# Optimization experiments

Hardware: AMD Instinct MI355X
Metric: run time of the kernel (lower is better)

## Reference

```python
import jax, jax.numpy as jnp
import numpy as np

ND, NT = 30000, 15000
FD, FT = 200, 570
H = 768
E_DD, E_DT, E_TT = 300000, 400000, 200000
NEG_SLOPE = 0.2


def _gat(x_src, x_dst, src, dst, Ws, Wd, a_s, a_d, b, n_dst):
    # PyG GATConv, heads=1: hs = lin_src(x_src), hd = lin_dst(x_dst)
    hs = x_src @ Ws                       # [Ns, H]
    hd = x_dst @ Wd                       # [Nd, H]
    es = hs @ a_s                         # [Ns]
    ed = hd @ a_d                         # [Nd]
    e = jax.nn.leaky_relu(es[src] + ed[dst], negative_slope=NEG_SLOPE)  # [E]
    m = jax.ops.segment_max(e, dst, num_segments=n_dst)
    m = jnp.where(jnp.isfinite(m), m, 0.0)
    w = jnp.exp(e - m[dst])
    s = jax.ops.segment_sum(w, dst, num_segments=n_dst)
    alpha = w / (s[dst] + 1e-16)
    out = jax.ops.segment_sum(hs[src] * alpha[:, None], dst, num_segments=n_dst)  # [n_dst, H]
    return out + b


def _layer(xd, xt, dd_src, dd_dst, dt_src, dt_dst, tt_src, tt_dst, p):
    nd, nt = xd.shape[0], xt.shape[0]
    sl_d = jnp.arange(nd, dtype=dd_src.dtype)
    sl_t = jnp.arange(nt, dtype=tt_src.dtype)
    # add_self_loops=True for the homogeneous relations d-d and t-t
    dds = jnp.concatenate([dd_src, sl_d]); ddd = jnp.concatenate([dd_dst, sl_d])
    tts = jnp.concatenate([tt_src, sl_t]); ttd = jnp.concatenate([tt_dst, sl_t])
    o_dd = _gat(xd, xd, dds, ddd, p['Wsrc_dd'], p['Wdst_dd'], p['asrc_dd'], p['adst_dd'], p['b_dd'], nd)
    o_rv = _gat(xt, xd, dt_dst, dt_src, p['Wsrc_rv'], p['Wdst_rv'], p['asrc_rv'], p['adst_rv'], p['b_rv'], nd)
    o_dt = _gat(xd, xt, dt_src, dt_dst, p['Wsrc_dt'], p['Wdst_dt'], p['asrc_dt'], p['adst_dt'], p['b_dt'], nt)
    o_tt = _gat(xt, xt, tts, ttd, p['Wsrc_tt'], p['Wdst_tt'], p['asrc_tt'], p['adst_tt'], p['b_tt'], nt)
    # HeteroConv aggr='sum', then relu per node type
    return jax.nn.relu(o_dd + o_rv), jax.nn.relu(o_dt + o_tt)


def setup_inputs() -> dict:
    key = jax.random.key(0)
    ks = jax.random.split(key, 40)
    d = {}
    d['drug_x'] = jax.random.normal(ks[0], (ND, FD), jnp.float32)
    d['target_x'] = jax.random.normal(ks[1], (NT, FT), jnp.float32)
    d['dd_src'] = jax.random.randint(ks[2], (E_DD,), 0, ND, jnp.int32)
    d['dd_dst'] = jax.random.randint(ks[3], (E_DD,), 0, ND, jnp.int32)
    d['dt_src'] = jax.random.randint(ks[4], (E_DT,), 0, ND, jnp.int32)
    d['dt_dst'] = jax.random.randint(ks[5], (E_DT,), 0, NT, jnp.int32)
    d['tt_src'] = jax.random.randint(ks[6], (E_TT,), 0, NT, jnp.int32)
    d['tt_dst'] = jax.random.randint(ks[7], (E_TT,), 0, NT, jnp.int32)
    d['drug_mask'] = jax.random.randint(ks[8], (ND, 1), 0, 2, jnp.int32)
    d['target_mask'] = jax.random.randint(ks[9], (NT, 1), 0, 2, jnp.int32)
    d['mask_drug'] = 0.05 * jax.random.normal(ks[10], (1, FD), jnp.float32)
    d['mask_target'] = 0.05 * jax.random.normal(ks[11], (1, FT), jnp.float32)
    i = 12
    for rel, fin_s, fin_d in [('dd', FD, FD), ('dt', FD, FT), ('rv', FT, FD), ('tt', FT, FT)]:
        d['Wsrc_' + rel] = 0.05 * jax.random.normal(ks[i], (fin_s, H), jnp.float32); i += 1
        d['Wdst_' + rel] = 0.05 * jax.random.normal(ks[i], (fin_d, H), jnp.float32); i += 1
        d['asrc_' + rel] = 0.05 * jax.random.normal(ks[i], (H,), jnp.float32); i += 1
        d['adst_' + rel] = 0.05 * jax.random.normal(ks[i], (H,), jnp.float32); i += 1
        d['b_' + rel] = jnp.zeros((H,), jnp.float32)
    return d


def reference(drug_x, target_x, dd_src, dd_dst, dt_src, dt_dst, tt_src, tt_dst,
              drug_mask, target_mask, mask_drug, mask_target,
              Wsrc_dd, Wdst_dd, asrc_dd, adst_dd, b_dd,
              Wsrc_dt, Wdst_dt, asrc_dt, adst_dt, b_dt,
              Wsrc_rv, Wdst_rv, asrc_rv, adst_rv, b_rv,
              Wsrc_tt, Wdst_tt, asrc_tt, adst_tt, b_tt):
    p = dict(Wsrc_dd=Wsrc_dd, Wdst_dd=Wdst_dd, asrc_dd=asrc_dd, adst_dd=adst_dd, b_dd=b_dd,
             Wsrc_dt=Wsrc_dt, Wdst_dt=Wdst_dt, asrc_dt=asrc_dt, adst_dt=adst_dt, b_dt=b_dt,
             Wsrc_rv=Wsrc_rv, Wdst_rv=Wdst_rv, asrc_rv=asrc_rv, adst_rv=adst_rv, b_rv=b_rv,
             Wsrc_tt=Wsrc_tt, Wdst_tt=Wdst_tt, asrc_tt=asrc_tt, adst_tt=adst_tt, b_tt=b_tt)
    xd, xt = _layer(drug_x, target_x, dd_src, dd_dst, dt_src, dt_dst, tt_src, tt_dst, p)
    # MAE branch: replace masked node features with learned mask token, rerun conv
    dm = drug_mask.astype(jnp.float32)
    tm = target_mask.astype(jnp.float32)
    _dx = drug_x * (1.0 - dm) + dm * mask_drug
    _tx = target_x * (1.0 - tm) + tm * mask_target
    _xd, _xt = _layer(_dx, _tx, dd_src, dd_dst, dt_src, dt_dst, tt_src, tt_dst, p)
    loss_mae = (((xd - _xd) ** 2) * dm).sum() / (dm.sum() * H + 1e-16) \
             + (((xt - _xt) ** 2) * tm).sum() / (tm.sum() * H + 1e-16)
    return (xd, xt, loss_mae)
```

## Files before the change

kernel.cpp:

```cpp
#include <hip/hip_runtime.h>
#include <hip/hip_bf16.h>

#define ND 30000
#define NT 15000
#define FD 200
#define FT 570
#define HDIM 768
#define EDD 300000
#define EDT 400000
#define ETT 200000

#define KPD 256
#define KPT 576
#define KPA 832

#define BM 128
#define BN 128
#define GBK 32
#define KTILES (KPA / GBK)
#define MTD ((ND + BM - 1) / BM)
#define MTT ((NT + BM - 1) / BM)

typedef __attribute__((ext_vector_type(8))) short short8;
typedef __attribute__((ext_vector_type(4))) float float4v;


__device__ __forceinline__ float ldx(const void* p, size_t i, int f32) {
  return f32 ? ((const float*)p)[i]
             : __bfloat162float(((const __hip_bfloat16*)p)[i]);
}
__device__ __forceinline__ void stx(void* p, size_t i, int f32, float v) {
  if (f32) ((float*)p)[i] = v;
  else     ((__hip_bfloat16*)p)[i] = __float2bfloat16(v);
}
__device__ __forceinline__ float b2f(unsigned short u) {
  return __uint_as_float(((unsigned)u) << 16);
}
__device__ __forceinline__ unsigned short f2b(float f) {
  __hip_bfloat16 h = __float2bfloat16(f);
  return *(unsigned short*)&h;
}
__device__ __forceinline__ unsigned pk2(float a, float b) {
  return (unsigned)f2b(a) | ((unsigned)f2b(b) << 16);
}

__device__ __forceinline__ float wave_reduce(float v) {
#pragma unroll
  for (int off = 32; off > 0; off >>= 1) v += __shfl_xor(v, off, 64);
  return v;
}

__global__ void sniff(const void* x, int* flag) {
  int t = threadIdx.x;
  float cnt = 0.f;
  for (int i = t; i < 8192; i += 256) {
    float v = __bfloat162float(((const __hip_bfloat16*)x)[i]);
    if (!(fabsf(v) < 100.f)) cnt += 1.f;
  }
  cnt = wave_reduce(cnt);
  __shared__ float red[4];
  if ((t & 63) == 0) red[t >> 6] = cnt;
  __syncthreads();
  if (t == 0) flag[0] = (red[0] + red[1] + red[2] + red[3] > 256.f) ? 1 : 0;
}

__global__ __launch_bounds__(256) void wa_dot8(
    const void* W0, const void* W1, const void* W2, const void* W3,
    const void* W4, const void* W5, const void* W6, const void* W7,
    const void* a0, const void* a1, const void* a2, const void* a3,
    const void* a4, const void* a5, const void* a6, const void* a7,
    float* __restrict__ vaD, float* __restrict__ vaT,
    const int* __restrict__ flag) {
  const void* Ws[8] = {W0, W1, W2, W3, W4, W5, W6, W7};
  const void* as[8] = {a0, a1, a2, a3, a4, a5, a6, a7};
  int f32 = flag[0];
  int wid = (blockIdx.x * 256 + threadIdx.x) >> 6;
  int lane = threadIdx.x & 63;
  const void* W; const void* a; float* out; int k;
  if (wid < 4 * FD) {
    int q = wid / FD; k = wid - q * FD;
    W = Ws[q]; a = as[q]; out = vaD + q * FD + k;
  } else {
    int w2 = wid - 4 * FD;
    if (w2 >= 4 * FT) return;
    int q = w2 / FT; k = w2 - q * FT;
    W = Ws[4 + q]; a = as[4 + q]; out = vaT + q * FT + k;
  }
  float acc = 0.f;
  for (int h = lane; h < HDIM; h += 64)
    acc += ldx(W, (size_t)k * HDIM + h, f32) * ldx(a, h, f32);
  acc = wave_reduce(acc);
  if (lane == 0) *out = acc;
}

__global__ void tok_dots(const void* __restrict__ tok1, const void* __restrict__ tok2,
                         const float* __restrict__ vaD, const float* __restrict__ vaT,
                         float* __restrict__ ts, const int* __restrict__ flag) {
  int w = threadIdx.x >> 6;
  int lane = threadIdx.x & 63;
  int f32 = flag[0];
  float acc = 0.f;
  if (w < 4) {
    for (int k = lane; k < FD; k += 64) acc += ldx(tok1, k, f32) * vaD[w * FD + k];
  } else {
    int q = w - 4;
    for (int k = lane; k < FT; k += 64) acc += ldx(tok2, k, f32) * vaT[q * FT + k];
  }
  acc = wave_reduce(acc);
  if (lane == 0) {
    const int map[8] = {0, 1, 3, 4, 2, 5, 6, 7};
    ts[map[w]] = acc;
  }
}

__global__ __launch_bounds__(256) void pack_rowdot(
    const void* __restrict__ xD, const void* __restrict__ xT,
    const float* __restrict__ vaD, const float* __restrict__ vaT,
    unsigned short* __restrict__ Ad, unsigned short* __restrict__ At,
    float* __restrict__ dvec, float* __restrict__ tvec,
    const int* __restrict__ flag) {
  int wid = (blockIdx.x * 256 + threadIdx.x) >> 6;
  int lane = threadIdx.x & 63;
  int f32 = flag[0];
  const void* x; const float* va; unsigned short* Aout; float* outv; int K, Kp, row;
  if (wid < ND) { x = xD; va = vaD; Aout = Ad; outv = dvec; K = FD; Kp = KPD; row = wid; }
  else if (wid < ND + NT) { x = xT; va = vaT; Aout = At; outv = tvec; K = FT; Kp = KPT; row = wid - ND; }
  else return;
  float a0 = 0.f, a1 = 0.f, a2 = 0.f, a3 = 0.f;
  for (int it = 0; it * 256 < Kp; ++it) {
    int base = 4 * lane + it * 256;
    if (base >= Kp) continue;
    ushort4 o;
    unsigned short r[4];
    float fv[4];
#pragma unroll
    for (int c = 0; c < 4; ++c) {
      int kk = base + c;
      float f = (kk < K) ? ldx(x, (size_t)row * K + kk, f32) : 0.f;
      fv[c] = f;
      r[c] = f2b(f);
    }
    o.x = r[0]; o.y = r[1]; o.z = r[2]; o.w = r[3];
    *(ushort4*)(Aout + (size_t)row * Kp + base) = o;
#pragma unroll
    for (int c = 0; c < 4; ++c) {
      int kk = base + c;
      if (kk < K) {
        a0 += fv[c] * va[kk];
        a1 += fv[c] * va[K + kk];
        a2 += fv[c] * va[2 * K + kk];
        a3 += fv[c] * va[3 * K + kk];
      }
    }
  }
  a0 = wave_reduce(a0); a1 = wave_reduce(a1);
  a2 = wave_reduce(a2); a3 = wave_reduce(a3);
  if (lane == 0) {
    float* o = outv + (size_t)row * 4;
    o[0] = a0; o[1] = a1; o[2] = a2; o[3] = a3;
  }
}

__global__ __launch_bounds__(256) void pack_bTa2(
    const void* __restrict__ W1a, const void* __restrict__ W2a, unsigned short* __restrict__ Ba,
    const void* __restrict__ W1b, const void* __restrict__ W2b, unsigned short* __restrict__ Bb,
    const int* __restrict__ flag) {
  int f32 = flag[0];
  long long one = (long long)HDIM * KPA / 4;
  long long gid = (long long)blockIdx.x * 256 + threadIdx.x;
  if (gid >= 2 * one) return;
  const void* W1; const void* W2; unsigned short* Bout;
  if (gid < one) { W1 = W1a; W2 = W2a; Bout = Ba; }
  else { W1 = W1b; W2 = W2b; Bout = Bb; gid -= one; }
  long long e0 = gid * 4;
  int n = (int)(e0 / KPA);
  int k = (int)(e0 % KPA);
  ushort4 o;
  unsigned short r[4];
#pragma unroll
  for (int c = 0; c < 4; ++c) {
    int kk = k + c;
    float f = 0.f;
    if (kk < 256) {
      if (kk < FD) f = ldx(W1, (size_t)kk * HDIM + n, f32);
    } else {
      int k2 = kk - 256;
      if (k2 < FT) f = ldx(W2, (size_t)k2 * HDIM + n, f32);
    }
    r[c] = f2b(f);
  }
  o.x = r[0]; o.y = r[1]; o.z = r[2]; o.w = r[3];
  *(ushort4*)(Bout + e0) = o;
}

__global__ void zero_i32(int* __restrict__ p, int n) {
  int i = blockIdx.x * 256 + threadIdx.x;
  if (i < n) p[i] = 0;
}

__global__ void count4(const int* __restrict__ dd_dst, const int* __restrict__ dt_src,
                       const int* __restrict__ dt_dst, const int* __restrict__ tt_dst,
                       int* __restrict__ c_dd, int* __restrict__ c_rv,
                       int* __restrict__ c_dt, int* __restrict__ c_tt) {
  int i = blockIdx.x * 256 + threadIdx.x;
  if (i < EDD + ND) { int d = (i < EDD) ? dd_dst[i] : i - EDD; atomicAdd(&c_dd[d], 1); return; }
  i -= EDD + ND;
  if (i < EDT) { atomicAdd(&c_rv[dt_src[i]], 1); return; }
  i -= EDT;
  if (i < EDT) { atomicAdd(&c_dt[dt_dst[i]], 1); return; }
  i -= EDT;
  if (i < ETT + NT) { int d = (i < ETT) ? tt_dst[i] : i - ETT; atomicAdd(&c_tt[d], 1); }
}

__global__ __launch_bounds__(256) void scan6(
    const int* __restrict__ a0, int n0, int* __restrict__ o0,
    const int* __restrict__ a1, int n1, int* __restrict__ o1,
    const int* __restrict__ a2, int n2, int* __restrict__ o2,
    const int* __restrict__ a3, int n3, int* __restrict__ o3,
    const int* __restrict__ a4, int n4, int* __restrict__ o4,
    const int* __restrict__ a5, int n5, int* __restrict__ o5) {
  const int* a; int n; int* o;
  switch (blockIdx.x) {
    case 0: a = a0; n = n0; o = o0; break;
    case 1: a = a1; n = n1; o = o1; break;
    case 2: a = a2; n = n2; o = o2; break;
    case 3: a = a3; n = n3; o = o3; break;
    case 4: a = a4; n = n4; o = o4; break;
    default: a = a5; n = n5; o = o5; break;
  }
  __shared__ int part[256];
  int t = threadIdx.x;
  int strip = (n + 255) / 256;
  int lo = min(t * strip, n), hi = min(lo + strip, n);
  int s = 0;
  for (int i = lo; i < hi; ++i) s += a[i];
  part[t] = s;
  __syncthreads();
  if (t == 0) {
    int run = 0;
    for (int i = 0; i < 256; ++i) { int v = part[i]; part[i] = run; run += v; }
  }
  __syncthreads();
  int run = part[t];
  for (int i = lo; i < hi; ++i) { o[i] = run; run += a[i]; }
  if (hi == n) o[n] = run;
}

__global__ void ridx2(const int* __restrict__ mD, const int* __restrict__ cD,
                      int* __restrict__ rD,
                      const int* __restrict__ mT, const int* __restrict__ cT,
                      int* __restrict__ rT) {
  int i = blockIdx.x * 256 + threadIdx.x;
  if (i < ND) { if (mD[i] != 0) rD[cD[i]] = i; return; }
  i -= ND;
  if (i < NT) { if (mT[i] != 0) rT[cT[i]] = i; }
}

__global__ void fill4(const int* __restrict__ dd_src, const int* __restrict__ dd_dst,
                      const int* __restrict__ dt_src, const int* __restrict__ dt_dst,
                      const int* __restrict__ tt_src, const int* __restrict__ tt_dst,
                      const int* __restrict__ rp_dd, int* __restrict__ f_dd, int* __restrict__ ei_dd,
                      const int* __restrict__ rp_rv, int* __restrict__ f_rv, int* __restrict__ ei_rv,
                      const int* __restrict__ rp_dt, int* __restrict__ f_dt, int* __restrict__ ei_dt,
                      const int* __restrict__ rp_tt, int* __restrict__ f_tt, int* __restrict__ ei_tt) {
  int i = blockIdx.x * 256 + threadIdx.x;
  if (i < EDD + ND) {
    int s, d;
    if (i < EDD) { s = dd_src[i]; d = dd_dst[i]; } else { s = d = i - EDD; }
    ei_dd[rp_dd[d] + atomicAdd(&f_dd[d], 1)] = s;
    return;
  }
  i -= EDD + ND;
  if (i < EDT) {
    int d = dt_src[i], s = dt_dst[i];
    ei_rv[rp_rv[d] + atomicAdd(&f_rv[d], 1)] = s;
    return;
  }
  i -= EDT;
  if (i < EDT) {
    int d = dt_dst[i], s = dt_src[i];
    ei_dt[rp_dt[d] + atomicAdd(&f_dt[d], 1)] = s;
    return;
  }
  i -= EDT;
  if (i < ETT + NT) {
    int s, d;
    if (i < ETT) { s = tt_src[i]; d = tt_dst[i]; } else { s = d = i - ETT; }
    ei_tt[rp_tt[d] + atomicAdd(&f_tt[d], 1)] = s;
  }
}

__device__ __forceinline__ void fma4(float* acc, uint2 A, float al) {
  unsigned w;
  w = A.x; acc[0] += al * __uint_as_float(w << 16); acc[1] += al * __uint_as_float(w & 0xffff0000u);
  w = A.y; acc[2] += al * __uint_as_float(w << 16); acc[3] += al * __uint_as_float(w & 0xffff0000u);
}

__device__ __forceinline__ float lrexp(float v) {
  v = (v >= 0.f) ? v : 0.2f * v;
  return __expf(v);
}

__global__ __launch_bounds__(256) void gat_agg2(
    const unsigned short* __restrict__ A1, const unsigned short* __restrict__ A2,
    const int* __restrict__ msk1, const int* __restrict__ msk2,
    const void* __restrict__ tok1, const void* __restrict__ tok2,
    const float* __restrict__ tokscal,
    const int* __restrict__ rpD1, const int* __restrict__ eiD1,
    const float* __restrict__ esD1, const float* __restrict__ edD1,
    const int* __restrict__ rpD2, const int* __restrict__ eiD2,
    const float* __restrict__ esD2, const float* __restrict__ edD2,
    const int* __restrict__ cidxD,
    unsigned short* __restrict__ aggd1, unsigned short* __restrict__ aggd2,
    const int* __restrict__ rpT1, const int* __restrict__ eiT1,
    const float* __restrict__ esT1, const float* __restrict__ edT1,
    const int* __restrict__ rpT2, const int* __restrict__ eiT2,
    const float* __restrict__ esT2, const float* __restrict__ edT2,
    const int* __restrict__ cidxT,
    unsigned short* __restrict__ aggt1, unsigned short* __restrict__ aggt2,
    const int* __restrict__ flag) {
  int gwid = (blockIdx.x * 256 + threadIdx.x) >> 6;
  int lane = threadIdx.x & 63;
  if (gwid >= ND + NT) return;
  int f32 = flag[0];

  const int *rp1, *ei1, *rp2, *ei2, *cidx;
  const float *es1, *ed1, *es2, *ed2, *ts;
  const int* mdst;
  unsigned short *agg1, *agg2;
  int wid;
  if (gwid < ND) {
    wid = gwid; mdst = msk1;
    rp1 = rpD1; ei1 = eiD1; es1 = esD1; ed1 = edD1;
    rp2 = rpD2; ei2 = eiD2; es2 = esD2; ed2 = edD2;
    cidx = cidxD; agg1 = aggd1; agg2 = aggd2; ts = tokscal;
  } else {
    wid = gwid - ND; mdst = msk2;
    rp1 = rpT1; ei1 = eiT1; es1 = esT1; ed1 = edT1;
    rp2 = rpT2; ei2 = eiT2; es2 = esT2; ed2 = edT2;
    cidx = cidxT; agg1 = aggt1; agg2 = aggt2; ts = tokscal + 4;
  }
// ... 75 lines not shown
      fma4(ac1 + 8, rb, a1);
      ac1[12] += a1 * b2f(rc);
      if (need2) {
        if (msk2[sn] != 0) {
          wt += lrexp(tes + ted) * i2;
        } else {
          float a2 = lrexp(ev + ted) * i2;
          fma4(ac2 + 4, ra, a2);
          fma4(ac2 + 8, rb, a2);
          ac2[12] += a2 * b2f(rc);
        }
      }
    }
    if (need2) {
#pragma unroll
      for (int c = 0; c < 4; ++c) {
        int colA = 4 * lane + c;
        int colB = 256 + 4 * lane + c;
        ac2[4 + c] += wt * ldx(tok2, colA, f32);
        ac2[8 + c] += wt * ldx(tok2, colB, f32);
      }
      int colC = 512 + lane;
      ac2[12] += wt * ((colC < FT) ? ldx(tok2, colC, f32) : 0.f);
    }
  }

  unsigned short* o1 = agg1 + (size_t)wid * KPA;
  uint2 u;
  u.x = pk2(ac1[0], ac1[1]);  u.y = pk2(ac1[2], ac1[3]);  *(uint2*)(o1 + 4 * lane) = u;
  u.x = pk2(ac1[4], ac1[5]);  u.y = pk2(ac1[6], ac1[7]);  *(uint2*)(o1 + 256 + 4 * lane) = u;
  u.x = pk2(ac1[8], ac1[9]);  u.y = pk2(ac1[10], ac1[11]); *(uint2*)(o1 + 512 + 4 * lane) = u;
  o1[768 + lane] = f2b(ac1[12]);
  if (need2) {
    unsigned short* o2 = agg2 + (size_t)cidx[wid] * KPA;
    u.x = pk2(ac2[0], ac2[1]);  u.y = pk2(ac2[2], ac2[3]);  *(uint2*)(o2 + 4 * lane) = u;
    u.x = pk2(ac2[4], ac2[5]);  u.y = pk2(ac2[6], ac2[7]);  *(uint2*)(o2 + 256 + 4 * lane) = u;
    u.x = pk2(ac2[8], ac2[9]);  u.y = pk2(ac2[10], ac2[11]); *(uint2*)(o2 + 512 + 4 * lane) = u;
    o2[768 + lane] = f2b(ac2[12]);
  }
}


__global__ __launch_bounds__(256) void gemm2(
    const unsigned short* __restrict__ A0, const unsigned short* __restrict__ B0,
    const void* __restrict__ c1_0, const void* __restrict__ c2_0,
    int M0s, const int* __restrict__ mc0, const int* __restrict__ rx0,
    unsigned long long base0, float* __restrict__ pp0,
    const unsigned short* __restrict__ A1, const unsigned short* __restrict__ B1,
    const void* __restrict__ c1_1, const void* __restrict__ c2_1,
    int M1s, const int* __restrict__ mc1, const int* __restrict__ rx1,
    unsigned long long base1, float* __restrict__ pp1,
    int mt0, int nwg, void* __restrict__ out, int mode,
    const int* __restrict__ flag) {
  __shared__ unsigned long long lds8[4096];
  unsigned short* ldsS = (unsigned short*)lds8;
  float* Cls = (float*)lds8;

  int b = blockIdx.x;
  int q = nwg >> 3, r = nwg & 7;
  int xcd = b & 7, pos = b >> 3;
  int wg = (xcd < r ? xcd * (q + 1) : r * (q + 1) + (xcd - r) * q) + pos;
  int prob = (wg >= 6 * mt0) ? 1 : 0;
  int rel = prob ? (wg - 6 * mt0) : wg;
  int mt = rel / 6, nt = rel - mt * 6;

  const unsigned short* A = prob ? A1 : A0;
  const unsigned short* Bt = prob ? B1 : B0;
  const void* c1 = prob ? c1_1 : c1_0;
  const void* c2 = prob ? c2_1 : c2_0;
  const int* mc = prob ? mc1 : mc0;
  const int* ridx = prob ? rx1 : rx0;
  size_t base = prob ? base1 : base0;
  float* parts = prob ? pp1 : pp0;
  int M = prob ? M1s : M0s;
  if (mc) M = *mc;
  int m0 = mt * BM;
  if (m0 >= M) return;
  int n0 = nt * BN;

  int t = threadIdx.x;
  int wave = t >> 6, lane = t & 63;
  int quad = lane >> 4, l15 = lane & 15;
  int wrow = (wave & 1) * 64, wcol = (wave >> 1) * 64;
  float4v acc[4][4];
#pragma unroll
  for (int i = 0; i < 4; ++i)
#pragma unroll
    for (int j = 0; j < 4; ++j) acc[i][j] = (float4v){0.f, 0.f, 0.f, 0.f};

  auto stage = [&](int buf, int k0) {
#pragma unroll
    for (int i = 0; i < 2; ++i) {
      int chunk = (wave * 2 + i) * 64 + lane;
      int row = chunk >> 2;
      int cs = (chunk & 3) ^ ((row >> 1) & 3);
      const unsigned short* ga = A + (size_t)(m0 + row) * KPA + k0 + cs * 8;
      __builtin_amdgcn_global_load_lds(
          (const __attribute__((address_space(1))) unsigned int*)ga,
          (__attribute__((address_space(3))) unsigned int*)(ldsS + buf * 4096 + (wave * 2 + i) * 512),
          16, 0, 0);
      const unsigned short* gb = Bt + (size_t)(n0 + row) * KPA + k0 + cs * 8;
      __builtin_amdgcn_global_load_lds(
          (const __attribute__((address_space(1))) unsigned int*)gb,
          (__attribute__((address_space(3))) unsigned int*)(ldsS + 8192 + buf * 4096 + (wave * 2 + i) * 512),
          16, 0, 0);
    }
  };
  auto compute = [&](int buf) {
    short8 a[4], bfr[4];
#pragma unroll
    for (int i = 0; i < 4; ++i) {
      int rr = wrow + i * 16 + l15;
      a[i] = *(const short8*)(ldsS + buf * 4096 + rr * 32 + ((quad ^ ((rr >> 1) & 3)) << 3));
    }
#pragma unroll
    for (int j = 0; j < 4; ++j) {
      int rc = wcol + j * 16 + l15;
      bfr[j] = *(const short8*)(ldsS + 8192 + buf * 4096 + rc * 32 + ((quad ^ ((rc >> 1) & 3)) << 3));
    }
#pragma unroll
    for (int i = 0; i < 4; ++i)
#pragma unroll
      for (int j = 0; j < 4; ++j)
        acc[i][j] = __builtin_amdgcn_mfma_f32_16x16x32_bf16(a[i], bfr[j], acc[i][j], 0, 0, 0);
  };

  stage(0, 0);
  int cur = 0;
#pragma unroll 1
  for (int ks = 1; ks < KTILES; ++ks) {
    stage(cur ^ 1, ks * GBK);
    asm volatile("s_waitcnt vmcnt(4)" ::: "memory");
    __builtin_amdgcn_sched_barrier(0);
    __builtin_amdgcn_s_barrier();
    compute(cur);
    __builtin_amdgcn_s_barrier();
    cur ^= 1;
  }
  asm volatile("s_waitcnt vmcnt(0)" ::: "memory");
  __builtin_amdgcn_sched_barrier(0);
  __builtin_amdgcn_s_barrier();
  compute(cur);

  int f32 = flag[0];
  float bias[4];
#pragma unroll
  for (int j = 0; j < 4; ++j) {
    int n = n0 + wcol + j * 16 + l15;
    bias[j] = ldx(c1, n, f32) + ldx(c2, n, f32);
  }
  float cpart = 0.f;
#pragma unroll
  for (int h = 0; h < 2; ++h) {
    __syncthreads();
    if ((wave >> 1) == h) {
#pragma unroll
      for (int i = 0; i < 4; ++i)
#pragma unroll
        for (int j = 0; j < 4; ++j)
#pragma unroll
          for (int rr = 0; rr < 4; ++rr) {
            int row = wrow + i * 16 + quad * 4 + rr;
            int col = (j * 16 + l15) ^ (((row >> 2) & 1) << 4);
            float v = acc[i][j][rr] + bias[j];
            Cls[row * 64 + col] = v > 0.f ? v : 0.f;
          }
    }
    __syncthreads();
#pragma unroll
    for (int i = 0; i < 8; ++i) {
      int ch = t + i * 256;
      int row = ch >> 4, cc = ch & 15;
      int m = m0 + row;
      if (m >= M) continue;
      int scc = cc ^ (((row >> 2) & 1) << 2);
      float4v v = *(const float4v*)(Cls + row * 64 + scc * 4);
      int n = n0 + h * 64 + cc * 4;
      if (mode == 1) {
        size_t idx = base + (size_t)m * HDIM + n;
        if (f32) {
          *(float4v*)((float*)out + idx) = v;
        } else {
          uint2 u; u.x = pk2(v[0], v[1]); u.y = pk2(v[2], v[3]);
          *(uint2*)((unsigned short*)out + idx) = u;
        }
      } else {
        int orig = ridx[m];
        size_t idx = base + (size_t)orig * HDIM + n;
        float d0, d1, d2, d3;
        if (f32) {
          float4v w = *(const float4v*)((const float*)out + idx);
          d0 = w[0] - v[0]; d1 = w[1] - v[1]; d2 = w[2] - v[2]; d3 = w[3] - v[3];
        } else {
          uint2 u = *(const uint2*)((const unsigned short*)out + idx);
          d0 = __uint_as_float(u.x << 16) - v[0];
// ... 56 lines not shown
  const void* b_dt    = d_in[21];
  const void* Wsrc_rv = d_in[22]; const void* Wdst_rv = d_in[23];
  const void* asrc_rv = d_in[24]; const void* adst_rv = d_in[25];
  const void* b_rv    = d_in[26];
  const void* Wsrc_tt = d_in[27]; const void* Wdst_tt = d_in[28];
  const void* asrc_tt = d_in[29]; const void* adst_tt = d_in[30];
  const void* b_tt    = d_in[31];

  char* p = (char*)d_ws;
  auto alloc = [&](size_t bytes) -> void* {
    void* r = (void*)p;
    p += (bytes + 255) & ~(size_t)255;
    return r;
  };
  const size_t PAD = (size_t)BM * KPA * 2;
  unsigned short* Ad    = (unsigned short*)alloc((size_t)ND * KPD * 2);
  unsigned short* At    = (unsigned short*)alloc((size_t)NT * KPT * 2);
  unsigned short* aggd1 = (unsigned short*)alloc((size_t)ND * KPA * 2 + PAD);
  unsigned short* aggd2 = (unsigned short*)alloc((size_t)ND * KPA * 2 + PAD);
  unsigned short* aggt1 = (unsigned short*)alloc((size_t)NT * KPA * 2 + PAD);
  unsigned short* aggt2 = (unsigned short*)alloc((size_t)NT * KPA * 2 + PAD);
  unsigned short* BdW   = (unsigned short*)alloc((size_t)HDIM * KPA * 2);
  unsigned short* BtW   = (unsigned short*)alloc((size_t)HDIM * KPA * 2);
  float* dvec1 = (float*)alloc((size_t)ND * 4 * 4);
  float* tvec1 = (float*)alloc((size_t)NT * 4 * 4);
  int* rp_dd = (int*)alloc((size_t)(ND + 1) * 4);
  int* rp_rv = (int*)alloc((size_t)(ND + 1) * 4);
  int* rp_dt = (int*)alloc((size_t)(NT + 1) * 4);
  int* rp_tt = (int*)alloc((size_t)(NT + 1) * 4);
  int* ei_dd = (int*)alloc((size_t)(EDD + ND) * 4);
  int* ei_rv = (int*)alloc((size_t)EDT * 4);
  int* ei_dt = (int*)alloc((size_t)EDT * 4);
  int* ei_tt = (int*)alloc((size_t)(ETT + NT) * 4);
  const int ZN = 4 * (ND + NT) + 4096;
  int* zblock = (int*)alloc((size_t)ZN * 4);
  int* cnt_dd = zblock;
  int* cnt_rv = cnt_dd + ND;
  int* cnt_dt = cnt_rv + ND;
  int* cnt_tt = cnt_dt + NT;
  int* f_dd   = cnt_tt + NT;
  int* f_rv   = f_dd + ND;
  int* f_dt   = f_rv + ND;
  int* f_tt   = f_dt + NT;
  float* parts = (float*)(f_tt + NT);
  int* cidxD = (int*)alloc((size_t)(ND + 1) * 4);
  int* cidxT = (int*)alloc((size_t)(NT + 1) * 4);
  int* ridxD = (int*)alloc((size_t)ND * 4);
  int* ridxT = (int*)alloc((size_t)NT * 4);
  float* vaD = (float*)alloc((size_t)4 * FD * 4);
  float* vaT = (float*)alloc((size_t)4 * FT * 4);
  float* tokscal = (float*)alloc(64);
  int*   flag  = (int*)alloc(256);

  sniff<<<1, 256, 0, stream>>>(drug_x, flag);
  zero_i32<<<(ZN + 255) / 256, 256, 0, stream>>>(zblock, ZN);

  {
    int waves = 4 * FD + 4 * FT;
    wa_dot8<<<(waves * 64 + 255) / 256, 256, 0, stream>>>(
        Wsrc_dd, Wdst_dd, Wdst_rv, Wsrc_dt, Wsrc_rv, Wdst_dt, Wsrc_tt, Wdst_tt,
        asrc_dd, adst_dd, adst_rv, asrc_dt, asrc_rv, adst_dt, asrc_tt, adst_tt,
        vaD, vaT, flag);
    tok_dots<<<1, 512, 0, stream>>>(mask_drug, mask_target, vaD, vaT, tokscal, flag);
  }

  {
    long long tb = 2 * ((long long)HDIM * KPA / 4);
    pack_bTa2<<<(int)((tb + 255) / 256), 256, 0, stream>>>(Wsrc_dd, Wsrc_rv, BdW,
                                                           Wsrc_dt, Wsrc_tt, BtW, flag);
  }

  {
    int total = (EDD + ND) + EDT + EDT + (ETT + NT);
    count4<<<(total + 255) / 256, 256, 0, stream>>>(dd_dst, dt_src, dt_dst, tt_dst,
                                                    cnt_dd, cnt_rv, cnt_dt, cnt_tt);
    scan6<<<6, 256, 0, stream>>>(cnt_dd, ND, rp_dd, cnt_rv, ND, rp_rv,
                                 cnt_dt, NT, rp_dt, cnt_tt, NT, rp_tt,
                                 drug_mask, ND, cidxD, target_mask, NT, cidxT);
    ridx2<<<(ND + NT + 255) / 256, 256, 0, stream>>>(drug_mask, cidxD, ridxD,
                                                     target_mask, cidxT, ridxT);
    fill4<<<(total + 255) / 256, 256, 0, stream>>>(dd_src, dd_dst, dt_src, dt_dst,
                                                   tt_src, tt_dst,
                                                   rp_dd, f_dd, ei_dd, rp_rv, f_rv, ei_rv,
                                                   rp_dt, f_dt, ei_dt, rp_tt, f_tt, ei_tt);
  }

  pack_rowdot<<<((ND + NT) * 64 + 255) / 256, 256, 0, stream>>>(
      drug_x, target_x, vaD, vaT, Ad, At, dvec1, tvec1, flag);

  gat_agg2<<<(ND + NT + 3) / 4, 256, 0, stream>>>(
      Ad, At, drug_mask, target_mask, mask_drug, mask_target, tokscal,
      rp_dd, ei_dd, dvec1 + 0, dvec1 + 1,
      rp_rv, ei_rv, tvec1 + 0, dvec1 + 2,
      cidxD, aggd1, aggd2,
      rp_dt, ei_dt, dvec1 + 3, tvec1 + 1,
      rp_tt, ei_tt, tvec1 + 2, tvec1 + 3,
      cidxT, aggt1, aggt2, flag);

  size_t baseT = (size_t)ND * HDIM;
  size_t baseL = baseT + (size_t)NT * HDIM;

  const int NWG = 6 * (MTD + MTT);
  gemm2<<<NWG, 256, 0, stream>>>(
      aggd1, BdW, b_dd, b_rv, ND, nullptr, nullptr, 0ULL, parts,
      aggt1, BtW, b_dt, b_tt, NT, nullptr, nullptr, (unsigned long long)baseT, parts,
      MTD, NWG, d_out, 1, flag);
  gemm2<<<NWG, 256, 0, stream>>>(
      aggd2, BdW, b_dd, b_rv, ND, cidxD + ND, ridxD, 0ULL, parts,
      aggt2, BtW, b_dt, b_tt, NT, cidxT + NT, ridxT, (unsigned long long)baseT, parts + 2048,
      MTD, NWG, d_out, 2, flag);

  loss_final<<<1, 256, 0, stream>>>(parts, cidxD + ND, cidxT + NT, d_out, baseL, flag);
}
```

Baseline: 918.1 us.

## Merge setup kernels into fewer launches and triple-buffer GEMM LDS pipeline

Folds the small preprocessing kernels (sniff, zeroing, counting, weight-vector dots, weight packing, scan, token dots, ridx, fill, row packing) into four combined launches whose blocks pick their role by index, cutting launch count and inter-kernel gaps. Separately, the GEMM main loop moves from double to triple buffering in LDS, prefetching two K-tiles ahead with adjusted vmcnt waits. The larger LDS footprint may lower GEMM occupancy. Merged kernels also place independent stages in one grid, so the heavy atomic and pack work now shares a launch.

```diff
diff --git a/kernel.cpp b/kernel.cpp
--- a/kernel.cpp
+++ b/kernel.cpp
@@ -21,6 +21,13 @@
 #define MTD ((ND + BM - 1) / BM)
 #define MTT ((NT + BM - 1) / BM)
 
+#define TOT_EDGE ((EDD + ND) + EDT + EDT + (ETT + NT))
+#define NB_CNT ((TOT_EDGE + 255) / 256)
+#define NB_WA (((4 * FD + 4 * FT) * 64 + 255) / 256)
+#define NB_PB ((2 * HDIM * KPA / 4 + 255) / 256)
+#define NB_RIDX ((ND + NT + 255) / 256)
+#define NB_PRD (((ND + NT) * 64 + 255) / 256)
+
 typedef __attribute__((ext_vector_type(8))) short short8;
 typedef __attribute__((ext_vector_type(4))) float float4v;
 
@@ -50,243 +57,253 @@
   return v;
 }
 
-__global__ void sniff(const void* x, int* flag) {
-  int t = threadIdx.x;
-  float cnt = 0.f;
-  for (int i = t; i < 8192; i += 256) {
-    float v = __bfloat162float(((const __hip_bfloat16*)x)[i]);
-    if (!(fabsf(v) < 100.f)) cnt += 1.f;
-  }
-  cnt = wave_reduce(cnt);
-  __shared__ float red[4];
-  if ((t & 63) == 0) red[t >> 6] = cnt;
-  __syncthreads();
-  if (t == 0) flag[0] = (red[0] + red[1] + red[2] + red[3] > 256.f) ? 1 : 0;
-}
-
-__global__ __launch_bounds__(256) void wa_dot8(
+__global__ __launch_bounds__(256) void init_k(const void* __restrict__ x,
+                                              int* __restrict__ flag,
+                                              int* __restrict__ zp, int zn) {
+  if (blockIdx.x == 0) {
+    int t = threadIdx.x;
+    float cnt = 0.f;
+    for (int i = t; i < 8192; i += 256) {
+      float v = __bfloat162float(((const __hip_bfloat16*)x)[i]);
+      if (!(fabsf(v) < 100.f)) cnt += 1.f;
+    }
+    cnt = wave_reduce(cnt);
+    __shared__ float red[4];
+    if ((t & 63) == 0) red[t >> 6] = cnt;
+    __syncthreads();
+    if (t == 0) flag[0] = (red[0] + red[1] + red[2] + red[3] > 256.f) ? 1 : 0;
+  } else {
+    int i = (blockIdx.x - 1) * 256 + threadIdx.x;
+    if (i < zn) zp[i] = 0;
+  }
+}
+
+__global__ __launch_bounds__(256) void setup_k(
+    const int* __restrict__ dd_dst, const int* __restrict__ dt_src,
+    const int* __restrict__ dt_dst, const int* __restrict__ tt_dst,
+    int* __restrict__ c_dd, int* __restrict__ c_rv,
+    int* __restrict__ c_dt, int* __restrict__ c_tt,
     const void* W0, const void* W1, const void* W2, const void* W3,
     const void* W4, const void* W5, const void* W6, const void* W7,
     const void* a0, const void* a1, const void* a2, const void* a3,
     const void* a4, const void* a5, const void* a6, const void* a7,
     float* __restrict__ vaD, float* __restrict__ vaT,
+    const void* __restrict__ PW1a, const void* __restrict__ PW2a, unsigned short* __restrict__ Ba,
+    const void* __restrict__ PW1b, const void* __restrict__ PW2b, unsigned short* __restrict__ Bb,
     const int* __restrict__ flag) {
-  const void* Ws[8] = {W0, W1, W2, W3, W4, W5, W6, W7};
-  const void* as[8] = {a0, a1, a2, a3, a4, a5, a6, a7};
-  int f32 = flag[0];
-  int wid = (blockIdx.x * 256 + threadIdx.x) >> 6;
-  int lane = threadIdx.x & 63;
-  const void* W; const void* a; float* out; int k;
-  if (wid < 4 * FD) {
-    int q = wid / FD; k = wid - q * FD;
-    W = Ws[q]; a = as[q]; out = vaD + q * FD + k;
+  int b = blockIdx.x;
+  if (b < NB_CNT) {
+    int i = b * 256 + threadIdx.x;
+    if (i < EDD + ND) { int d = (i < EDD) ? dd_dst[i] : i - EDD; atomicAdd(&c_dd[d], 1); return; }
+    i -= EDD + ND;
+    if (i < EDT) { atomicAdd(&c_rv[dt_src[i]], 1); return; }
+    i -= EDT;
+    if (i < EDT) { atomicAdd(&c_dt[dt_dst[i]], 1); return; }
+    i -= EDT;
+    if (i < ETT + NT) { int d = (i < ETT) ? tt_dst[i] : i - ETT; atomicAdd(&c_tt[d], 1); }
+    return;
+  }
+  b -= NB_CNT;
+  if (b < NB_WA) {
+    const void* Ws[8] = {W0, W1, W2, W3, W4, W5, W6, W7};
+    const void* as[8] = {a0, a1, a2, a3, a4, a5, a6, a7};
+    int f32 = flag[0];
+    int wid = (b * 256 + threadIdx.x) >> 6;
+    int lane = threadIdx.x & 63;
+    const void* W; const void* a; float* out; int k;
+    if (wid < 4 * FD) {
+      int q = wid / FD; k = wid - q * FD;
+      W = Ws[q]; a = as[q]; out = vaD + q * FD + k;
+    } else {
+      int w2 = wid - 4 * FD;
+      if (w2 >= 4 * FT) return;
+      int q = w2 / FT; k = w2 - q * FT;
+      W = Ws[4 + q]; a = as[4 + q]; out = vaT + q * FT + k;
+    }
+    float acc = 0.f;
+    for (int h = lane; h < HDIM; h += 64)
+      acc += ldx(W, (size_t)k * HDIM + h, f32) * ldx(a, h, f32);
+    acc = wave_reduce(acc);
+    if (lane == 0) *out = acc;
+    return;
+  }
+  b -= NB_WA;
+  {
+    int f32 = flag[0];
+    long long one = (long long)HDIM * KPA / 4;
+    long long gid = (long long)b * 256 + threadIdx.x;
+    if (gid >= 2 * one) return;
+    const void* Wp1; const void* Wp2; unsigned short* Bout;
+    if (gid < one) { Wp1 = PW1a; Wp2 = PW2a; Bout = Ba; }
+    else { Wp1 = PW1b; Wp2 = PW2b; Bout = Bb; gid -= one; }
+    long long e0 = gid * 4;
+    int n = (int)(e0 / KPA);
+    int k = (int)(e0 % KPA);
+    ushort4 o;
+    unsigned short r[4];
+#pragma unroll
+    for (int c = 0; c < 4; ++c) {
+      int kk = k + c;
+      float f = 0.f;
+      if (kk < 256) {
+        if (kk < FD) f = ldx(Wp1, (size_t)kk * HDIM + n, f32);
+      } else {
+        int k2 = kk - 256;
+        if (k2 < FT) f = ldx(Wp2, (size_t)k2 * HDIM + n, f32);
+      }
+      r[c] = f2b(f);
+    }
+    o.x = r[0]; o.y = r[1]; o.z = r[2]; o.w = r[3];
+    *(ushort4*)(Bout + e0) = o;
+  }
+}
+
+__global__ __launch_bounds__(256) void scan_tok_k(
+    const int* __restrict__ a0, int n0, int* __restrict__ o0,
+    const int* __restrict__ a1, int n1, int* __restrict__ o1,
+    const int* __restrict__ a2, int n2, int* __restrict__ o2,
+    const int* __restrict__ a3, int n3, int* __restrict__ o3,
+    const int* __restrict__ a4, int n4, int* __restrict__ o4,
+    const int* __restrict__ a5, int n5, int* __restrict__ o5,
+    const void* __restrict__ tok1, const void* __restrict__ tok2,
+    const float* __restrict__ vaD, const float* __restrict__ vaT,
+    float* __restrict__ ts, const int* __restrict__ flag) {
+  __shared__ int part[256];
+  if (blockIdx.x < 6) {
+    const int* a; int n; int* o;
+    switch (blockIdx.x) {
+      case 0: a = a0; n = n0; o = o0; break;
+      case 1: a = a1; n = n1; o = o1; break;
+      case 2: a = a2; n = n2; o = o2; break;
+      case 3: a = a3; n = n3; o = o3; break;
+      case 4: a = a4; n = n4; o = o4; break;
+      default: a = a5; n = n5; o = o5; break;
+    }
+    int t = threadIdx.x;
+    int strip = (n + 255) / 256;
+    int lo = min(t * strip, n), hi = min(lo + strip, n);
+    int s = 0;
+    for (int i = lo; i < hi; ++i) s += a[i];
+    part[t] = s;
+    __syncthreads();
+    if (t == 0) {
+      int run = 0;
+      for (int i = 0; i < 256; ++i) { int v = part[i]; part[i] = run; run += v; }
+    }
+    __syncthreads();
+    int run = part[t];
+    for (int i = lo; i < hi; ++i) { o[i] = run; run += a[i]; }
+    if (hi == n) o[n] = run;
   } else {
-    int w2 = wid - 4 * FD;
-    if (w2 >= 4 * FT) return;
-    int q = w2 / FT; k = w2 - q * FT;
-    W = Ws[4 + q]; a = as[4 + q]; out = vaT + q * FT + k;
-  }
-  float acc = 0.f;
-  for (int h = lane; h < HDIM; h += 64)
-    acc += ldx(W, (size_t)k * HDIM + h, f32) * ldx(a, h, f32);
-  acc = wave_reduce(acc);
-  if (lane == 0) *out = acc;
-}
-
-__global__ void tok_dots(const void* __restrict__ tok1, const void* __restrict__ tok2,
-                         const float* __restrict__ vaD, const float* __restrict__ vaT,
-                         float* __restrict__ ts, const int* __restrict__ flag) {
-  int w = threadIdx.x >> 6;
-  int lane = threadIdx.x & 63;
-  int f32 = flag[0];
-  float acc = 0.f;
-  if (w < 4) {
+    int w = threadIdx.x >> 6, lane = threadIdx.x & 63;
+    int f32 = flag[0];
+    const int mapD[4] = {0, 1, 3, 4};
+    const int mapT[4] = {2, 5, 6, 7};
+    float acc = 0.f;
     for (int k = lane; k < FD; k += 64) acc += ldx(tok1, k, f32) * vaD[w * FD + k];
-  } else {
-    int q = w - 4;
-    for (int k = lane; k < FT; k += 64) acc += ldx(tok2, k, f32) * vaT[q * FT + k];
-  }
-  acc = wave_reduce(acc);
-  if (lane == 0) {
-    const int map[8] = {0, 1, 3, 4, 2, 5, 6, 7};
-    ts[map[w]] = acc;
-  }
-}
-
-__global__ __launch_bounds__(256) void pack_rowdot(
+    acc = wave_reduce(acc);
+    if (lane == 0) ts[mapD[w]] = acc;
+    acc = 0.f;
+    for (int k = lane; k < FT; k += 64) acc += ldx(tok2, k, f32) * vaT[w * FT + k];
+    acc = wave_reduce(acc);
+    if (lane == 0) ts[mapT[w]] = acc;
+  }
+}
+
+__global__ __launch_bounds__(256) void build_k(
+    const int* __restrict__ dd_src, const int* __restrict__ dd_dst,
+    const int* __restrict__ dt_src, const int* __restrict__ dt_dst,
+    const int* __restrict__ tt_src, const int* __restrict__ tt_dst,
+    const int* __restrict__ rp_dd, int* __restrict__ f_dd, int* __restrict__ ei_dd,
+    const int* __restrict__ rp_rv, int* __restrict__ f_rv, int* __restrict__ ei_rv,
+    const int* __restrict__ rp_dt, int* __restrict__ f_dt, int* __restrict__ ei_dt,
+    const int* __restrict__ rp_tt, int* __restrict__ f_tt, int* __restrict__ ei_tt,
+    const int* __restrict__ mD, const int* __restrict__ cD, int* __restrict__ rD,
+    const int* __restrict__ mT, const int* __restrict__ cT, int* __restrict__ rT,
     const void* __restrict__ xD, const void* __restrict__ xT,
     const float* __restrict__ vaD, const float* __restrict__ vaT,
     unsigned short* __restrict__ Ad, unsigned short* __restrict__ At,
     float* __restrict__ dvec, float* __restrict__ tvec,
     const int* __restrict__ flag) {
-  int wid = (blockIdx.x * 256 + threadIdx.x) >> 6;
-  int lane = threadIdx.x & 63;
-  int f32 = flag[0];
-  const void* x; const float* va; unsigned short* Aout; float* outv; int K, Kp, row;
-  if (wid < ND) { x = xD; va = vaD; Aout = Ad; outv = dvec; K = FD; Kp = KPD; row = wid; }
-  else if (wid < ND + NT) { x = xT; va = vaT; Aout = At; outv = tvec; K = FT; Kp = KPT; row = wid - ND; }
-  else return;
-  float a0 = 0.f, a1 = 0.f, a2 = 0.f, a3 = 0.f;
-  for (int it = 0; it * 256 < Kp; ++it) {
-    int base = 4 * lane + it * 256;
-    if (base >= Kp) continue;
-    ushort4 o;
-    unsigned short r[4];
-    float fv[4];
-#pragma unroll
-    for (int c = 0; c < 4; ++c) {
-      int kk = base + c;
-      float f = (kk < K) ? ldx(x, (size_t)row * K + kk, f32) : 0.f;
-      fv[c] = f;
-      r[c] = f2b(f);
-    }
-    o.x = r[0]; o.y = r[1]; o.z = r[2]; o.w = r[3];
-    *(ushort4*)(Aout + (size_t)row * Kp + base) = o;
-#pragma unroll
-    for (int c = 0; c < 4; ++c) {
-      int kk = base + c;
-      if (kk < K) {
-        a0 += fv[c] * va[kk];
-        a1 += fv[c] * va[K + kk];
-        a2 += fv[c] * va[2 * K + kk];
-        a3 += fv[c] * va[3 * K + kk];
-      }
-    }
-  }
-  a0 = wave_reduce(a0); a1 = wave_reduce(a1);
-  a2 = wave_reduce(a2); a3 = wave_reduce(a3);
-  if (lane == 0) {
-    float* o = outv + (size_t)row * 4;
-    o[0] = a0; o[1] = a1; o[2] = a2; o[3] = a3;
-  }
-}
-
-__global__ __launch_bounds__(256) void pack_bTa2(
-    const void* __restrict__ W1a, const void* __restrict__ W2a, unsigned short* __restrict__ Ba,
-    const void* __restrict__ W1b, const void* __restrict__ W2b, unsigned short* __restrict__ Bb,
-    const int* __restrict__ flag) {
-  int f32 = flag[0];
-  long long one = (long long)HDIM * KPA / 4;
-  long long gid = (long long)blockIdx.x * 256 + threadIdx.x;
-  if (gid >= 2 * one) return;
-  const void* W1; const void* W2; unsigned short* Bout;
-  if (gid < one) { W1 = W1a; W2 = W2a; Bout = Ba; }
-  else { W1 = W1b; W2 = W2b; Bout = Bb; gid -= one; }
-  long long e0 = gid * 4;
-  int n = (int)(e0 / KPA);
-  int k = (int)(e0 % KPA);
-  ushort4 o;
-  unsigned short r[4];
-#pragma unroll
-  for (int c = 0; c < 4; ++c) {
-    int kk = k + c;
-    float f = 0.f;
-    if (kk < 256) {
-      if (kk < FD) f = ldx(W1, (size_t)kk * HDIM + n, f32);
-    } else {
-      int k2 = kk - 256;
-      if (k2 < FT) f = ldx(W2, (size_t)k2 * HDIM + n, f32);
-    }
-    r[c] = f2b(f);
-  }
-  o.x = r[0]; o.y = r[1]; o.z = r[2]; o.w = r[3];
-  *(ushort4*)(Bout + e0) = o;
-}
-
-__global__ void zero_i32(int* __restrict__ p, int n) {
-  int i = blockIdx.x * 256 + threadIdx.x;
-  if (i < n) p[i] = 0;
-}
-
-__global__ void count4(const int* __restrict__ dd_dst, const int* __restrict__ dt_src,
-                       const int* __restrict__ dt_dst, const int* __restrict__ tt_dst,
-                       int* __restrict__ c_dd, int* __restrict__ c_rv,
-                       int* __restrict__ c_dt, int* __restrict__ c_tt) {
-  int i = blockIdx.x * 256 + threadIdx.x;
-  if (i < EDD + ND) { int d = (i < EDD) ? dd_dst[i] : i - EDD; atomicAdd(&c_dd[d], 1); return; }
-  i -= EDD + ND;
-  if (i < EDT) { atomicAdd(&c_rv[dt_src[i]], 1); return; }
-  i -= EDT;
-  if (i < EDT) { atomicAdd(&c_dt[dt_dst[i]], 1); return; }
-  i -= EDT;
-  if (i < ETT + NT) { int d = (i < ETT) ? tt_dst[i] : i - ETT; atomicAdd(&c_tt[d], 1); }
-}
-
-__global__ __launch_bounds__(256) void scan6(
-    const int* __restrict__ a0, int n0, int* __restrict__ o0,
-    const int* __restrict__ a1, int n1, int* __restrict__ o1,
-    const int* __restrict__ a2, int n2, int* __restrict__ o2,
-    const int* __restrict__ a3, int n3, int* __restrict__ o3,
-    const int* __restrict__ a4, int n4, int* __restrict__ o4,
-    const int* __restrict__ a5, int n5, int* __restrict__ o5) {
-  const int* a; int n; int* o;
-  switch (blockIdx.x) {
-    case 0: a = a0; n = n0; o = o0; break;
-    case 1: a = a1; n = n1; o = o1; break;
-    case 2: a = a2; n = n2; o = o2; break;
-    case 3: a = a3; n = n3; o = o3; break;
-    case 4: a = a4; n = n4; o = o4; break;
-    default: a = a5; n = n5; o = o5; break;
-  }
-  __shared__ int part[256];
-  int t = threadIdx.x;
-  int strip = (n + 255) / 256;
-  int lo = min(t * strip, n), hi = min(lo + strip, n);
-  int s = 0;
-  for (int i = lo; i < hi; ++i) s += a[i];
-  part[t] = s;
-  __syncthreads();
-  if (t == 0) {
-    int run = 0;
-    for (int i = 0; i < 256; ++i) { int v = part[i]; part[i] = run; run += v; }
-  }
-  __syncthreads();
-  int run = part[t];
-  for (int i = lo; i < hi; ++i) { o[i] = run; run += a[i]; }
-  if (hi == n) o[n] = run;
-}
-
-__global__ void ridx2(const int* __restrict__ mD, const int* __restrict__ cD,
-                      int* __restrict__ rD,
-                      const int* __restrict__ mT, const int* __restrict__ cT,
-                      int* __restrict__ rT) {
-  int i = blockIdx.x * 256 + threadIdx.x;
-  if (i < ND) { if (mD[i] != 0) rD[cD[i]] = i; return; }
-  i -= ND;
-  if (i < NT) { if (mT[i] != 0) rT[cT[i]] = i; }
-}
-
-__global__ void fill4(const int* __restrict__ dd_src, const int* __restrict__ dd_dst,
-                      const int* __restrict__ dt_src, const int* __restrict__ dt_dst,
-                      const int* __restrict__ tt_src, const int* __restrict__ tt_dst,
-                      const int* __restrict__ rp_dd, int* __restrict__ f_dd, int* __restrict__ ei_dd,
-                      const int* __restrict__ rp_rv, int* __restrict__ f_rv, int* __restrict__ ei_rv,
-                      const int* __restrict__ rp_dt, int* __restrict__ f_dt, int* __restrict__ ei_dt,
-                      const int* __restrict__ rp_tt, int* __restrict__ f_tt, int* __restrict__ ei_tt) {
-  int i = blockIdx.x * 256 + threadIdx.x;
-  if (i < EDD + ND) {
-    int s, d;
-    if (i < EDD) { s = dd_src[i]; d = dd_dst[i]; } else { s = d = i - EDD; }
-    ei_dd[rp_dd[d] + atomicAdd(&f_dd[d], 1)] = s;
+  int b = blockIdx.x;
+  if (b < NB_CNT) {
+    int i = b * 256 + threadIdx.x;
+    if (i < EDD + ND) {
+      int s, d;
+      if (i < EDD) { s = dd_src[i]; d = dd_dst[i]; } else { s = d = i - EDD; }
+      ei_dd[rp_dd[d] + atomicAdd(&f_dd[d], 1)] = s;
+      return;
+    }
+    i -= EDD + ND;
+    if (i < EDT) {
+      int d = dt_src[i], s = dt_dst[i];
+      ei_rv[rp_rv[d] + atomicAdd(&f_rv[d], 1)] = s;
+      return;
+    }
+    i -= EDT;
+    if (i < EDT) {
+      int d = dt_dst[i], s = dt_src[i];
+      ei_dt[rp_dt[d] + atomicAdd(&f_dt[d], 1)] = s;
+      return;
+    }
+    i -= EDT;
+    if (i < ETT + NT) {
+      int s, d;
+      if (i < ETT) { s = tt_src[i]; d = tt_dst[i]; } else { s = d = i - ETT; }
+      ei_tt[rp_tt[d] + atomicAdd(&f_tt[d], 1)] = s;
+    }
     return;
   }
-  i -= EDD + ND;
-  if (i < EDT) {
-    int d = dt_src[i], s = dt_dst[i];
-    ei_rv[rp_rv[d] + atomicAdd(&f_rv[d], 1)] = s;
+  b -= NB_CNT;
+  if (b < NB_RIDX) {
+    int i = b * 256 + threadIdx.x;
+    if (i < ND) { if (mD[i] != 0) rD[cD[i]] = i; return; }
+    i -= ND;
+    if (i < NT) { if (mT[i] != 0) rT[cT[i]] = i; }
     return;
   }
-  i -= EDT;
-  if (i < EDT) {
-    int d = dt_dst[i], s = dt_src[i];
-    ei_dt[rp_dt[d] + atomicAdd(&f_dt[d], 1)] = s;
-    return;
-  }
-  i -= EDT;
-  if (i < ETT + NT) {
-    int s, d;
-    if (i < ETT) { s = tt_src[i]; d = tt_dst[i]; } else { s = d = i - ETT; }
-    ei_tt[rp_tt[d] + atomicAdd(&f_tt[d], 1)] = s;
+  b -= NB_RIDX;
+  {
+    int wid = (b * 256 + threadIdx.x) >> 6;
+    int lane = threadIdx.x & 63;
+    int f32 = flag[0];
+    const void* x; const float* va; unsigned short* Aout; float* outv; int K, Kp, row;
+    if (wid < ND) { x = xD; va = vaD; Aout = Ad; outv = dvec; K = FD; Kp = KPD; row = wid; }
+    else if (wid < ND + NT) { x = xT; va = vaT; Aout = At; outv = tvec; K = FT; Kp = KPT; row = wid - ND; }
+    else return;
+    float s0 = 0.f, s1 = 0.f, s2 = 0.f, s3 = 0.f;
+    for (int it = 0; it * 256 < Kp; ++it) {
+      int base = 4 * lane + it * 256;
+      if (base >= Kp) continue;
+      ushort4 o;
+      unsigned short r[4];
+      float fv[4];
+#pragma unroll
+      for (int c = 0; c < 4; ++c) {
+        int kk = base + c;
+        float f = (kk < K) ? ldx(x, (size_t)row * K + kk, f32) : 0.f;
+        fv[c] = f;
+        r[c] = f2b(f);
+      }
+      o.x = r[0]; o.y = r[1]; o.z = r[2]; o.w = r[3];
+      *(ushort4*)(Aout + (size_t)row * Kp + base) = o;
+#pragma unroll
+      for (int c = 0; c < 4; ++c) {
+        int kk = base + c;
+        if (kk < K) {
+          s0 += fv[c] * va[kk];
+          s1 += fv[c] * va[K + kk];
+          s2 += fv[c] * va[2 * K + kk];
+          s3 += fv[c] * va[3 * K + kk];
+        }
+      }
+    }
+    s0 = wave_reduce(s0); s1 = wave_reduce(s1);
+    s2 = wave_reduce(s2); s3 = wave_reduce(s3);
+    if (lane == 0) {
+      float* o = outv + (size_t)row * 4;
+      o[0] = s0; o[1] = s1; o[2] = s2; o[3] = s3;
+    }
   }
 }
 
@@ -468,7 +485,7 @@
     unsigned long long base1, float* __restrict__ pp1,
     int mt0, int nwg, void* __restrict__ out, int mode,
     const int* __restrict__ flag) {
-  __shared__ unsigned long long lds8[4096];
+  __shared__ unsigned long long lds8[6144];
   unsigned short* ldsS = (unsigned short*)lds8;
   float* Cls = (float*)lds8;
 
@@ -518,7 +535,7 @@
       const unsigned short* gb = Bt + (size_t)(n0 + row) * KPA + k0 + cs * 8;
       __builtin_amdgcn_global_load_lds(
           (const __attribute__((address_space(1))) unsigned int*)gb,
-          (__attribute__((address_space(3))) unsigned int*)(ldsS + 8192 + buf * 4096 + (wave * 2 + i) * 512),
+          (__attribute__((address_space(3))) unsigned int*)(ldsS + 12288 + buf * 4096 + (wave * 2 + i) * 512),
           16, 0, 0);
     }
   };
@@ -532,7 +549,7 @@
 #pragma unroll
     for (int j = 0; j < 4; ++j) {
       int rc = wcol + j * 16 + l15;
-      bfr[j] = *(const short8*)(ldsS + 8192 + buf * 4096 + rc * 32 + ((quad ^ ((rc >> 1) & 3)) << 3));
+      bfr[j] = *(const short8*)(ldsS + 12288 + buf * 4096 + rc * 32 + ((quad ^ ((rc >> 1) & 3)) << 3));
     }
 #pragma unroll
     for (int i = 0; i < 4; ++i)
@@ -542,21 +559,25 @@
   };
 
   stage(0, 0);
-  int cur = 0;
+  stage(1, GBK);
 #pragma unroll 1
-  for (int ks = 1; ks < KTILES; ++ks) {
-    stage(cur ^ 1, ks * GBK);
-    asm volatile("s_waitcnt vmcnt(4)" ::: "memory");
+  for (int ks = 0; ks < KTILES - 2; ++ks) {
+    stage((ks + 2) % 3, (ks + 2) * GBK);
+    asm volatile("s_waitcnt vmcnt(8)" ::: "memory");
     __builtin_amdgcn_sched_barrier(0);
     __builtin_amdgcn_s_barrier();
-    compute(cur);
+    compute(ks % 3);
     __builtin_amdgcn_s_barrier();
-    cur ^= 1;
-  }
+  }
+  asm volatile("s_waitcnt vmcnt(4)" ::: "memory");
+  __builtin_amdgcn_sched_barrier(0);
+  __builtin_amdgcn_s_barrier();
+  compute((KTILES - 2) % 3);
+  __builtin_amdgcn_s_barrier();
   asm volatile("s_waitcnt vmcnt(0)" ::: "memory");
   __builtin_amdgcn_sched_barrier(0);
   __builtin_amdgcn_s_barrier();
-  compute(cur);
+  compute((KTILES - 1) % 3);
 
   int f32 = flag[0];
   float bias[4];
@@ -719,40 +740,26 @@
   float* tokscal = (float*)alloc(64);
   int*   flag  = (int*)alloc(256);
 
-  sniff<<<1, 256, 0, stream>>>(drug_x, flag);
-  zero_i32<<<(ZN + 255) / 256, 256, 0, stream>>>(zblock, ZN);
-
-  {
-    int waves = 4 * FD + 4 * FT;
-    wa_dot8<<<(waves * 64 + 255) / 256, 256, 0, stream>>>(
-        Wsrc_dd, Wdst_dd, Wdst_rv, Wsrc_dt, Wsrc_rv, Wdst_dt, Wsrc_tt, Wdst_tt,
-        asrc_dd, adst_dd, adst_rv, asrc_dt, asrc_rv, adst_dt, asrc_tt, adst_tt,
-        vaD, vaT, flag);
-    tok_dots<<<1, 512, 0, stream>>>(mask_drug, mask_target, vaD, vaT, tokscal, flag);
-  }
-
-  {
-    long long tb = 2 * ((long long)HDIM * KPA / 4);
-    pack_bTa2<<<(int)((tb + 255) / 256), 256, 0, stream>>>(Wsrc_dd, Wsrc_rv, BdW,
-                                                           Wsrc_dt, Wsrc_tt, BtW, flag);
-  }
-
-  {
-    int total = (EDD + ND) + EDT + EDT + (ETT + NT);
-    count4<<<(total + 255) / 256, 256, 0, stream>>>(dd_dst, dt_src, dt_dst, tt_dst,
-                                                    cnt_dd, cnt_rv, cnt_dt, cnt_tt);
-    scan6<<<6, 256, 0, stream>>>(cnt_dd, ND, rp_dd, cnt_rv, ND, rp_rv,
-                                 cnt_dt, NT, rp_dt, cnt_tt, NT, rp_tt,
-                                 drug_mask, ND, cidxD, target_mask, NT, cidxT);
-    ridx2<<<(ND + NT + 255) / 256, 256, 0, stream>>>(drug_mask, cidxD, ridxD,
-                                                     target_mask, cidxT, ridxT);
-    fill4<<<(total + 255) / 256, 256, 0, stream>>>(dd_src, dd_dst, dt_src, dt_dst,
-                                                   tt_src, tt_dst,
-                                                   rp_dd, f_dd, ei_dd, rp_rv, f_rv, ei_rv,
-                                                   rp_dt, f_dt, ei_dt, rp_tt, f_tt, ei_tt);
-  }
-
-  pack_rowdot<<<((ND + NT) * 64 + 255) / 256, 256, 0, stream>>>(
+  init_k<<<1 + (ZN + 255) / 256, 256, 0, stream>>>(drug_x, flag, zblock, ZN);
+
+  setup_k<<<NB_CNT + NB_WA + NB_PB, 256, 0, stream>>>(
+      dd_dst, dt_src, dt_dst, tt_dst, cnt_dd, cnt_rv, cnt_dt, cnt_tt,
+      Wsrc_dd, Wdst_dd, Wdst_rv, Wsrc_dt, Wsrc_rv, Wdst_dt, Wsrc_tt, Wdst_tt,
+      asrc_dd, adst_dd, adst_rv, asrc_dt, asrc_rv, adst_dt, asrc_tt, adst_tt,
+      vaD, vaT,
+      Wsrc_dd, Wsrc_rv, BdW, Wsrc_dt, Wsrc_tt, BtW, flag);
+
+  scan_tok_k<<<7, 256, 0, stream>>>(
+      cnt_dd, ND, rp_dd, cnt_rv, ND, rp_rv,
+      cnt_dt, NT, rp_dt, cnt_tt, NT, rp_tt,
+      drug_mask, ND, cidxD, target_mask, NT, cidxT,
+      mask_drug, mask_target, vaD, vaT, tokscal, flag);
+
+  build_k<<<NB_CNT + NB_RIDX + NB_PRD, 256, 0, stream>>>(
+      dd_src, dd_dst, dt_src, dt_dst, tt_src, tt_dst,
+      rp_dd, f_dd, ei_dd, rp_rv, f_rv, ei_rv,
+      rp_dt, f_dt, ei_dt, rp_tt, f_tt, ei_tt,
+      drug_mask, cidxD, ridxD, target_mask, cidxT, ridxT,
       drug_x, target_x, vaD, vaT, Ad, At, dvec1, tvec1, flag);
 
   gat_agg2<<<(ND + NT + 3) / 4, 256, 0, stream>>>(
```

Result: faster. 889.0 us (-3.2%).
